# Kernel optimization log

Hardware: AMD Instinct MI355X
Metric: run time of the kernel (lower is better)

The kernel has to match this reference:

```python
import jax, jax.numpy as jnp
import numpy as np

B, H, F, T = 256, 1024, 512, 128  # batch, state_size, num_feature, num_predict

def setup_inputs() -> dict:
    key = jax.random.key(0)
    ks = jax.random.split(key, 8)
    s = 1.0 / np.sqrt(H)
    return {
        "x0": jax.random.normal(ks[0], (B, H), jnp.float32),
        "h0": jax.random.normal(ks[1], (B, H), jnp.float32),
        "c0": jax.random.normal(ks[2], (B, H), jnp.float32),
        "W": jax.random.uniform(ks[3], (H, 4 * H), jnp.float32, -s, s),   # input kernel (i,f,g,o)
        "U": jax.random.uniform(ks[4], (H, 4 * H), jnp.float32, -s, s),   # recurrent kernel
        "b": jnp.zeros((4 * H,), jnp.float32),
        "Wd": jax.random.uniform(ks[5], (H, F), jnp.float32, -s, s),      # Dense emission
        "bd": jnp.zeros((F,), jnp.float32),
    }

def _lstm_scan(x0, h0, c0, W, U, b):
    def step(carry, _):
        x, h, c = carry
        z = x @ W + h @ U + b                      # [B, 4H], Keras gate order i,f,g,o
        i, f, g, o = jnp.split(z, 4, axis=-1)
        c_new = jax.nn.sigmoid(f) * c + jax.nn.sigmoid(i) * jnp.tanh(g)
        h_new = jax.nn.sigmoid(o) * jnp.tanh(c_new)
        return (h_new, h_new, c_new), h_new       # output feeds back as next input
    (_, _, _), outs = jax.lax.scan(step, (x0, h0, c0), None, length=T)
    return outs                                    # [T, B, H]

def reference(x0, h0, c0, W, U, b, Wd, bd):
    outs = _lstm_scan(x0, h0, c0, W, U, b)         # [T, B, H]
    seq = jnp.transpose(outs, (1, 0, 2))           # [B, T, H]
    return seq @ Wd + bd                           # [B, T, F]
```

## Files before the change

### kernel.cpp

```cpp
#include <hip/hip_runtime.h>
#include <cstddef>
#include <cstdint>

typedef unsigned short ushort_t;
typedef __attribute__((ext_vector_type(8))) short bf16x8;
typedef __attribute__((ext_vector_type(4))) float f32x4;

#define Bb 256
#define Hh 1024
#define Ff 512
#define Tt 128

__device__ __forceinline__ ushort_t f2bf(float f) {
    unsigned int u = __float_as_uint(f);
    unsigned int r = (u + 0x7FFFu + ((u >> 16) & 1u)) >> 16;
    return (ushort_t)r;
}
__device__ __forceinline__ float sigf(float x)  { return 1.0f / (1.0f + __expf(-x)); }
__device__ __forceinline__ float tanhf_(float x){ return 2.0f / (1.0f + __expf(-2.0f * x)) - 1.0f; }

__device__ __forceinline__ void lds_barrier() {
    asm volatile("s_waitcnt lgkmcnt(0)" ::: "memory");
    __builtin_amdgcn_s_barrier();
    asm volatile("" ::: "memory");
}

__global__ void swz(const float* __restrict__ s0, const float* __restrict__ s1,
                    ushort_t* __restrict__ dst, int K, int N, int mode, int total)
{
    int KB = K >> 5;
    for (int idx = blockIdx.x * blockDim.x + threadIdx.x; idx < total;
         idx += gridDim.x * blockDim.x) {
        int blk   = idx >> 9;
        int lane  = (idx >> 3) & 63;
        int j     = idx & 7;
        int ntile = blk / KB;
        int kstep = blk - ntile * KB;
        int k = (kstep << 5) + ((lane >> 4) << 3) + j;
        int n;
        if (mode == 2) n = (ntile << 4) + (lane & 15);
        else           n = ((ntile & 3) << 10) + ((ntile >> 2) << 4) + (lane & 15);
        float v;
        if (mode == 0)      v = s0[(size_t)k * N + n] + s1[(size_t)k * N + n];
        else if (mode == 1) v = (k < 1024) ? s0[(size_t)k * N + n]
                                           : s1[(size_t)(k - 1024) * N + n];
        else                v = s0[(size_t)k * N + n];
        dst[idx] = f2bf(v);
    }
}

__global__ void mk_a0(const float* __restrict__ x0, const float* __restrict__ h0,
                      ushort_t* __restrict__ a0)
{
    int idx = blockIdx.x * blockDim.x + threadIdx.x;
    if (idx >= Bb * 2048) return;
    int r = idx >> 11, k = idx & 2047;
    float v = (k < 1024) ? x0[r * 1024 + k] : h0[r * 1024 + k - 1024];
    a0[idx] = f2bf(v);
}

__global__ void zero_bar(int* bar) {
    int i = blockIdx.x * blockDim.x + threadIdx.x;
    if (i < 1024) bar[i] = 0;
}


__global__ __launch_bounds__(256) void lstm_step(
    const ushort_t* __restrict__ Ap, int K,
    const ushort_t* __restrict__ Bw,
    const float* cin, float* cout,
    ushort_t* __restrict__ seqt,
    const float* __restrict__ bias)
{
    __shared__ __align__(16) ushort_t lA[32 * 512];
    __shared__ __align__(16) ushort_t lB[32 * 512];

    const int tid = threadIdx.x, w = tid >> 6, lane = tid & 63;
    const int id = blockIdx.x;
    const int ntg = ((id & 7) << 3) | (id >> 5);
    const int bt  = (id >> 3) & 3;
    const int r0 = bt << 6, hb = ntg << 4;
    const int wr = w >> 1, wc = w & 1;
    const int KB = K >> 5;

    f32x4 acc[2][2];
    #pragma unroll
    for (int m = 0; m < 2; ++m)
        #pragma unroll
        for (int n = 0; n < 2; ++n) acc[m][n] = (f32x4){0.f, 0.f, 0.f, 0.f};

    const int kp = tid & 31;
    const int q_a = kp & 3, kk_a = kp >> 2;

    for (int kc = 0; kc < K; kc += 256) {
        bf16x8 va[8];
        #pragma unroll
        for (int i = 0; i < 8; ++i) {
            int row = (i << 3) + (tid >> 5);
            va[i] = *(const bf16x8*)(Ap + (size_t)(r0 + row) * K + kc + (kp << 3));
        }
        bf16x8 vb[8];
        #pragma unroll
        for (int i = 0; i < 8; ++i)
            vb[i] = *(const bf16x8*)(Bw +
                ((((size_t)((ntg << 2) + w)) * KB + (kc >> 5) + i) << 9) + (lane << 3));
        #pragma unroll
        for (int i = 0; i < 8; ++i) {
            int row = (i << 3) + (tid >> 5);
            int msub = row >> 4, mm = row & 15;
            int pos = (q_a << 4) | (mm ^ (((kk_a << 2) + q_a) & 15));
            *(bf16x8*)&lA[((((kk_a << 2) + msub) << 6) + pos) << 3] = va[i];
        }
        #pragma unroll
        for (int i = 0; i < 8; ++i)
            *(bf16x8*)&lB[(((i << 2) + w) << 9) + (lane << 3)] = vb[i];
        __syncthreads();

        #pragma unroll
        for (int kk = 0; kk < 8; ++kk) {
            const int qq = lane >> 4, mm = lane & 15;
            const int pos = (qq << 4) | (mm ^ (((kk << 2) + qq) & 15));
            bf16x8 af[2], bfr[2];
            #pragma unroll
            for (int m = 0; m < 2; ++m)
                af[m] = *(const bf16x8*)&lA[((((kk << 2) + (wr << 1) + m) << 6) + pos) << 3];
            #pragma unroll
            for (int n = 0; n < 2; ++n)
                bfr[n] = *(const bf16x8*)&lB[((((kk << 2) + (wc << 1) + n) << 6) + lane) << 3];
            #pragma unroll
            for (int m = 0; m < 2; ++m)
                #pragma unroll
                for (int n = 0; n < 2; ++n)
                    acc[m][n] = __builtin_amdgcn_mfma_f32_16x16x32_bf16(
                        af[m], bfr[n], acc[m][n], 0, 0, 0);
        }
        __syncthreads();
    }

    float* lZ = (float*)lA;
    {
        int q = lane >> 4, nl = lane & 15;
        #pragma unroll
        for (int m = 0; m < 2; ++m)
            #pragma unroll
            for (int n = 0; n < 2; ++n)
                #pragma unroll
                for (int r = 0; r < 4; ++r)
                    lZ[((wr << 5) + (m << 4) + (q << 2) + r) * 68 +
                       (wc << 5) + (n << 4) + nl] = acc[m][n][r];
    }
    __syncthreads();

    #pragma unroll
    for (int i = 0; i < 4; ++i) {
        int idx = (i << 8) + tid;
        int row = idx >> 4, u = idx & 15;
        float zi = lZ[row * 68 +      u] + bias[       hb + u];
        float zf = lZ[row * 68 + 16 + u] + bias[1024 + hb + u];
        float zg = lZ[row * 68 + 32 + u] + bias[2048 + hb + u];
        float zo = lZ[row * 68 + 48 + u] + bias[3072 + hb + u];
        size_t cidx = (size_t)(r0 + row) * Hh + hb + u;
        float cp = cin[cidx];
        float cn = sigf(zf) * cp + sigf(zi) * tanhf_(zg);
        cout[cidx] = cn;
        seqt[cidx] = f2bf(sigf(zo) * tanhf_(cn));
    }
}

__global__ __launch_bounds__(256, 1) void lstm_scan(
    ushort_t* __restrict__ seq,
    const ushort_t* __restrict__ Msum,
    const float* __restrict__ bias,
    const float* __restrict__ cin,
    int* __restrict__ bar)
{
    __shared__ __align__(16) ushort_t lA[8][4096];

    const int tid = threadIdx.x, w = tid >> 6, lane = tid & 63;
    const int id = blockIdx.x;
    const int g  = id & 7;
    const int s  = id >> 3;
    const int r0 = g << 5;
    const int hb = s << 5;
    int* const barw = &bar[g << 5];

    bf16x8 Brg[2][32];
    #pragma unroll
    for (int n = 0; n < 2; ++n) {
        const int ntl = (w << 1) + n;
        const int gnt = (((s << 1) + (ntl >> 2)) << 2) + (ntl & 3);
        const ushort_t* bp = Msum + (((size_t)gnt << 5) << 9) + (lane << 3);
        #pragma unroll
        for (int ks = 0; ks < 32; ++ks) {
            Brg[n][ks] = *(const bf16x8*)(bp + ((size_t)ks << 9));
            asm volatile("" : "+a"(Brg[n][ks]));
        }
    }

    const int grow = tid >> 3, gu4 = (tid & 7) << 2;
    float c_reg[4], bi[4], bfv[4], bgv[4], bo[4];
    #pragma unroll
    for (int j = 0; j < 4; ++j) {
        int u = gu4 + j;
        c_reg[j] = cin[(size_t)(r0 + grow) * Hh + hb + u];
        bi[j]  = bias[       hb + u];
        bfv[j] = bias[1024 + hb + u];
        bgv[j] = bias[2048 + hb + u];
        bo[j]  = bias[3072 + hb + u];
    }

    float* lZ = (float*)lA;

    const int kp  = tid & 15;
    const int q_a = kp & 3, kk_a = kp >> 2;
    const int mm_s  = tid >> 4;
    const int pos_s = (q_a << 4) | (mm_s ^ (((kk_a << 2) + q_a) & 15));
    const int lw0   = (((kk_a << 1) << 6) | pos_s) << 3;
    const size_t ga0 = (size_t)(r0 + mm_s) * Hh + (kp << 3);

    #pragma unroll 1
    for (int t = 1; t < Tt; ++t) {
        const ushort_t* Ap = seq + ((size_t)(t - 1) << 18) + ga0;

        f32x4 acc[2][2];
        #pragma unroll
        for (int m = 0; m < 2; ++m)
            #pragma unroll
            for (int n = 0; n < 2; ++n) acc[m][n] = (f32x4){0.f, 0.f, 0.f, 0.f};

        bf16x8 rA[8][2];
        #pragma unroll
        for (int c = 0; c < 8; ++c)
            #pragma unroll
            for (int i = 0; i < 2; ++i)
                rA[c][i] = *(const bf16x8*)(Ap + (i << 14) + (c << 7));

        #pragma unroll
        for (int c = 0; c < 8; ++c)
            #pragma unroll
            for (int i = 0; i < 2; ++i)
                *(bf16x8*)&lA[c][lw0 + (i << 9)] = rA[c][i];
        lds_barrier();

        {
            const int qq = lane >> 4, mr = lane & 15;
            #pragma unroll
            for (int kc = 0; kc < 8; ++kc) {
                const ushort_t* lAc = lA[kc];
                #pragma unroll
                for (int kk = 0; kk < 4; ++kk) {
                    const int pos = (qq << 4) | (mr ^ (((kk << 2) + qq) & 15));
                    const int ks = (kc << 2) + kk;
                    bf16x8 af0 = *(const bf16x8*)&lAc[((((kk << 1) + 0) << 6) | pos) << 3];
                    bf16x8 af1 = *(const bf16x8*)&lAc[((((kk << 1) + 1) << 6) | pos) << 3];
                    acc[0][0] = __builtin_amdgcn_mfma_f32_16x16x32_bf16(af0, Brg[0][ks], acc[0][0], 0, 0, 0);
                    acc[0][1] = __builtin_amdgcn_mfma_f32_16x16x32_bf16(af0, Brg[1][ks], acc[0][1], 0, 0, 0);
                    acc[1][0] = __builtin_amdgcn_mfma_f32_16x16x32_bf16(af1, Brg[0][ks], acc[1][0], 0, 0, 0);
                    acc[1][1] = __builtin_amdgcn_mfma_f32_16x16x32_bf16(af1, Brg[1][ks], acc[1][1], 0, 0, 0);
                }
            }
        }
        lds_barrier();

        {
            const int q = lane >> 4, nl = lane & 15;
            #pragma unroll
            for (int m = 0; m < 2; ++m)
                #pragma unroll
                for (int n = 0; n < 2; ++n)
                    #pragma unroll
                    for (int r = 0; r < 4; ++r) {
                        int row = (m << 4) + (q << 2) + r;
                        int col = (((w << 1) + n) << 4) + nl;
                        lZ[(row << 7) + ((col + row * 5) & 127)] = acc[m][n][r];
                    }
        }
        lds_barrier();

        {
            const int rb5 = grow * 5;
            unsigned long long pk = 0;
            #pragma unroll
            for (int j = 0; j < 4; ++j) {
                int u = gu4 + j;
                int cb = ((u >> 4) << 6) + (u & 15);
                float zi = lZ[(grow << 7) + ((cb      + rb5) & 127)] + bi[j];
                float zf = lZ[(grow << 7) + ((cb + 16 + rb5) & 127)] + bfv[j];
                float zg = lZ[(grow << 7) + ((cb + 32 + rb5) & 127)] + bgv[j];
                float zo = lZ[(grow << 7) + ((cb + 48 + rb5) & 127)] + bo[j];
                float cn = sigf(zf) * c_reg[j] + sigf(zi) * tanhf_(zg);
                c_reg[j] = cn;
                pk |= (unsigned long long)f2bf(sigf(zo) * tanhf_(cn)) << (j << 4);
            }
            __hip_atomic_exchange(
                (unsigned long long*)&seq[((size_t)t << 18) +
                                          (size_t)(r0 + grow) * Hh + hb + gu4],
                pk, __ATOMIC_RELAXED, __HIP_MEMORY_SCOPE_AGENT);
        }

        if (t < Tt - 1) {
            __syncthreads();
            if (tid == 0) {
                __hip_atomic_fetch_add(barw, 1, __ATOMIC_RELAXED,
                                       __HIP_MEMORY_SCOPE_AGENT);
                int guard = 0;
                while (__hip_atomic_fetch_add(barw, 0, __ATOMIC_RELAXED,
                                              __HIP_MEMORY_SCOPE_AGENT) < (t << 5)
                       && ++guard < 30000)
                    __builtin_amdgcn_s_sleep(2);
            }
            lds_barrier();
        }
    }
}

__global__ __launch_bounds__(256) void emit(
    const ushort_t* __restrict__ seq,
    const ushort_t* __restrict__ Wsw,
    const float* __restrict__ bd,
    float* __restrict__ out)
{
    __shared__ __align__(16) ushort_t lA[2 * 8 * 64 * 8];
    __shared__ __align__(16) ushort_t lB[2 * 8 * 64 * 8];
    const int tid = threadIdx.x, w = tid >> 6, lane = tid & 63;
    const int id = blockIdx.x;
    const int rt = ((id >> 5) << 3) | (id & 7);
    const int ct = (id >> 3) & 3;
    const int r0 = rt << 7, f0 = ct << 7;
    const int wr = w >> 1, wc = w & 1;

    f32x4 acc[4][4];
    #pragma unroll
    for (int m = 0; m < 4; ++m)
        #pragma unroll
        for (int n = 0; n < 4; ++n) acc[m][n] = (f32x4){0.f, 0.f, 0.f, 0.f};

    for (int kc = 0; kc < Hh; kc += 64) {
        #pragma unroll
        for (int i = 0; i < 4; ++i) {
            int p = (i << 8) + tid;
            int row = p >> 3, kpp = p & 7;
            bf16x8 v = *(const bf16x8*)(seq + (size_t)(r0 + row) * Hh + kc + (kpp << 3));
            int kk = kpp >> 2, q = kpp & 3, msub = row >> 4, mm = row & 15;
            int pos = (q << 4) | (mm ^ (((kk << 2) + q) & 15));
            *(bf16x8*)&lA[((((kk << 3) + msub) << 6) + pos) << 3] = v;
        }
        #pragma unroll
        for (int i = 0; i < 4; ++i) {
            int d = (i << 8) + tid;
            int kk = d >> 9, csub = (d >> 6) & 7, ln = d & 63;
            int nt = (ct << 3) + csub;
            bf16x8 v = *(const bf16x8*)(Wsw + (((size_t)(nt * 32 + (kc >> 5) + kk)) << 9) + (ln << 3));
            *(bf16x8*)&lB[d << 3] = v;
        }
        __syncthreads();
        const int qq = lane >> 4, mm = lane & 15;
        #pragma unroll
        for (int kk = 0; kk < 2; ++kk) {
            const int pos = (qq << 4) | (mm ^ (((kk << 2) + qq) & 15));
            bf16x8 af[4], bfr[4];
            #pragma unroll
            for (int m = 0; m < 4; ++m)
                af[m] = *(const bf16x8*)&lA[((((kk << 3) + (wr << 2) + m) << 6) + pos) << 3];
            #pragma unroll
            for (int n = 0; n < 4; ++n)
                bfr[n] = *(const bf16x8*)&lB[((((kk << 3) + (wc << 2) + n) << 6) + lane) << 3];
            #pragma unroll
            for (int m = 0; m < 4; ++m)
                #pragma unroll
                for (int n = 0; n < 4; ++n)
                    acc[m][n] = __builtin_amdgcn_mfma_f32_16x16x32_bf16(
                        af[m], bfr[n], acc[m][n], 0, 0, 0);
        }
        __syncthreads();
    }

    int q = lane >> 4, nl = lane & 15;
    float bdv[4];
    #pragma unroll
    for (int n = 0; n < 4; ++n) bdv[n] = bd[f0 + (wc << 6) + (n << 4) + nl];
    #pragma unroll
    for (int m = 0; m < 4; ++m)
        #pragma unroll
        for (int r = 0; r < 4; ++r) {
            int grow2 = r0 + (wr << 6) + (m << 4) + (q << 2) + r;
            int tt = grow2 >> 8, bb = grow2 & 255;
            float* op = out + ((size_t)((bb << 7) + tt) << 9);
            #pragma unroll
            for (int n = 0; n < 4; ++n)
                op[f0 + (wc << 6) + (n << 4) + nl] = acc[m][n][r] + bdv[n];
        }
}

extern "C" void kernel_launch(void* const* d_in, const int* in_sizes, int n_in,
                              void* d_out, int out_size, void* d_ws, size_t ws_size,
                              hipStream_t stream)
{
    const float* x0 = (const float*)d_in[0];
    const float* h0 = (const float*)d_in[1];
    const float* c0 = (const float*)d_in[2];
    const float* W  = (const float*)d_in[3];
    const float* U  = (const float*)d_in[4];
    const float* b  = (const float*)d_in[5];
    const float* Wd = (const float*)d_in[6];
    const float* bd = (const float*)d_in[7];
    float* out = (float*)d_out;

    const size_t OFF_MCAT = 0;
    const size_t OFF_MSUM = 16777216;
    const size_t OFF_WSW  = 25165824;
    const size_t OFF_A0   = 26214400;
    const size_t OFF_SEQ  = 27262976;
    const size_t OFF_BAR  = 94371840;
    const size_t WS_NEED  = 94375936;
    if (ws_size < WS_NEED) return;

    char* ws = (char*)d_ws;
    ushort_t* Mcat = (ushort_t*)(ws + OFF_MCAT);
    ushort_t* Msum = (ushort_t*)(ws + OFF_MSUM);
    ushort_t* Wsw  = (ushort_t*)(ws + OFF_WSW);
    ushort_t* A0   = (ushort_t*)(ws + OFF_A0);
    ushort_t* seq  = (ushort_t*)(ws + OFF_SEQ);
    int*      bar  = (int*)(ws + OFF_BAR);
    float* cws = out;

    zero_bar<<<4, 256, 0, stream>>>(bar);
    mk_a0<<<2048, 256, 0, stream>>>(x0, h0, A0);
    swz<<<4096, 256, 0, stream>>>(W, U, Mcat, 2048, 4096, 1, 2048 * 4096);
    swz<<<2048, 256, 0, stream>>>(W, U, Msum, 1024, 4096, 0, 1024 * 4096);
    swz<<<512, 256, 0, stream>>>(Wd, nullptr, Wsw, 1024, 512, 2, 1024 * 512);

    lstm_step<<<256, 256, 0, stream>>>(A0, 2048, Mcat, c0, cws, seq, b);
    lstm_scan<<<256, 256, 0, stream>>>(seq, Msum, b, cws, bar);

    emit<<<1024, 256, 0, stream>>>(seq, Wsw, bd, out);
}
```

Baseline: 727.2 us.

## Split recurrent GEMM over K across waves and reduce partials in LDS

Each wave now covers all eight N tiles for one quarter of the K dimension instead of two N tiles over the full K. Partial sums go to a separate per-wave LDS region, and the gate epilogue adds the four partials with vectorized f32x4 loads. Because the partial buffer no longer aliases the A tile, the barrier between the MFMA loop and the partial write is removed. In exchange the kernel uses 64KB more LDS, does an extra reduction pass, and holds more accumulator registers per wave.

New measurement: 751.4 us. +3.3%, slower.

```diff
diff --git a/kernel.cpp b/kernel.cpp
--- a/kernel.cpp
+++ b/kernel.cpp
@@ -175,6 +175,7 @@
     int* __restrict__ bar)
 {
     __shared__ __align__(16) ushort_t lA[8][4096];
+    __shared__ __align__(16) float    lZp[16384];
 
     const int tid = threadIdx.x, w = tid >> 6, lane = tid & 63;
     const int id = blockIdx.x;
@@ -184,16 +185,15 @@
     const int hb = s << 5;
     int* const barw = &bar[g << 5];
 
-    bf16x8 Brg[2][32];
-    #pragma unroll
-    for (int n = 0; n < 2; ++n) {
-        const int ntl = (w << 1) + n;
+    bf16x8 Brg[8][8];
+    #pragma unroll
+    for (int ntl = 0; ntl < 8; ++ntl) {
         const int gnt = (((s << 1) + (ntl >> 2)) << 2) + (ntl & 3);
-        const ushort_t* bp = Msum + (((size_t)gnt << 5) << 9) + (lane << 3);
-        #pragma unroll
-        for (int ks = 0; ks < 32; ++ks) {
-            Brg[n][ks] = *(const bf16x8*)(bp + ((size_t)ks << 9));
-            asm volatile("" : "+a"(Brg[n][ks]));
+        const ushort_t* bp = Msum + (((size_t)((gnt << 5) + (w << 3))) << 9) + (lane << 3);
+        #pragma unroll
+        for (int kl = 0; kl < 8; ++kl) {
+            Brg[ntl][kl] = *(const bf16x8*)(bp + ((size_t)kl << 9));
+            asm volatile("" : "+a"(Brg[ntl][kl]));
         }
     }
 
@@ -209,8 +209,6 @@
         bo[j]  = bias[3072 + hb + u];
     }
 
-    float* lZ = (float*)lA;
-
     const int kp  = tid & 15;
     const int q_a = kp & 3, kk_a = kp >> 2;
     const int mm_s  = tid >> 4;
@@ -218,15 +216,18 @@
     const int lw0   = (((kk_a << 1) << 6) | pos_s) << 3;
     const size_t ga0 = (size_t)(r0 + mm_s) * Hh + (kp << 3);
 
+    const int cb = ((gu4 >> 4) << 6) + (gu4 & 15);
+    const int rb4 = grow << 2;
+
     #pragma unroll 1
     for (int t = 1; t < Tt; ++t) {
         const ushort_t* Ap = seq + ((size_t)(t - 1) << 18) + ga0;
 
-        f32x4 acc[2][2];
+        f32x4 acc[2][8];
         #pragma unroll
         for (int m = 0; m < 2; ++m)
             #pragma unroll
-            for (int n = 0; n < 2; ++n) acc[m][n] = (f32x4){0.f, 0.f, 0.f, 0.f};
+            for (int ntl = 0; ntl < 8; ++ntl) acc[m][ntl] = (f32x4){0.f, 0.f, 0.f, 0.f};
 
         bf16x8 rA[8][2];
         #pragma unroll
@@ -245,49 +246,53 @@
         {
             const int qq = lane >> 4, mr = lane & 15;
             #pragma unroll
-            for (int kc = 0; kc < 8; ++kc) {
-                const ushort_t* lAc = lA[kc];
+            for (int kl = 0; kl < 8; ++kl) {
+                const int kk = kl & 3;
+                const ushort_t* lAc = lA[(w << 1) + (kl >> 2)];
+                const int pos = (qq << 4) | (mr ^ (((kk << 2) + qq) & 15));
+                bf16x8 af0 = *(const bf16x8*)&lAc[((((kk << 1) + 0) << 6) | pos) << 3];
+                bf16x8 af1 = *(const bf16x8*)&lAc[((((kk << 1) + 1) << 6) | pos) << 3];
                 #pragma unroll
-                for (int kk = 0; kk < 4; ++kk) {
-                    const int pos = (qq << 4) | (mr ^ (((kk << 2) + qq) & 15));
-                    const int ks = (kc << 2) + kk;
-                    bf16x8 af0 = *(const bf16x8*)&lAc[((((kk << 1) + 0) << 6) | pos) << 3];
-                    bf16x8 af1 = *(const bf16x8*)&lAc[((((kk << 1) + 1) << 6) | pos) << 3];
-                    acc[0][0] = __builtin_amdgcn_mfma_f32_16x16x32_bf16(af0, Brg[0][ks], acc[0][0], 0, 0, 0);
-                    acc[0][1] = __builtin_amdgcn_mfma_f32_16x16x32_bf16(af0, Brg[1][ks], acc[0][1], 0, 0, 0);
-                    acc[1][0] = __builtin_amdgcn_mfma_f32_16x16x32_bf16(af1, Brg[0][ks], acc[1][0], 0, 0, 0);
-                    acc[1][1] = __builtin_amdgcn_mfma_f32_16x16x32_bf16(af1, Brg[1][ks], acc[1][1], 0, 0, 0);
+                for (int ntl = 0; ntl < 8; ++ntl) {
+                    acc[0][ntl] = __builtin_amdgcn_mfma_f32_16x16x32_bf16(af0, Brg[ntl][kl], acc[0][ntl], 0, 0, 0);
+                    acc[1][ntl] = __builtin_amdgcn_mfma_f32_16x16x32_bf16(af1, Brg[ntl][kl], acc[1][ntl], 0, 0, 0);
                 }
             }
         }
-        lds_barrier();
 
         {
             const int q = lane >> 4, nl = lane & 15;
+            float* zw = &lZp[w << 12];
             #pragma unroll
             for (int m = 0; m < 2; ++m)
                 #pragma unroll
-                for (int n = 0; n < 2; ++n)
+                for (int ntl = 0; ntl < 8; ++ntl)
                     #pragma unroll
                     for (int r = 0; r < 4; ++r) {
                         int row = (m << 4) + (q << 2) + r;
-                        int col = (((w << 1) + n) << 4) + nl;
-                        lZ[(row << 7) + ((col + row * 5) & 127)] = acc[m][n][r];
+                        int col = (ntl << 4) + nl;
+                        zw[(row << 7) + ((col + (row << 2)) & 127)] = acc[m][ntl][r];
                     }
         }
         lds_barrier();
 
         {
-            const int rb5 = grow * 5;
+            f32x4 vi = (f32x4){0.f,0.f,0.f,0.f}, vf = vi, vg = vi, vo = vi;
+            #pragma unroll
+            for (int p = 0; p < 4; ++p) {
+                const float* zp = &lZp[(p << 12) + (grow << 7)];
+                vi += *(const f32x4*)&zp[(cb      + rb4) & 127];
+                vf += *(const f32x4*)&zp[(cb + 16 + rb4) & 127];
+                vg += *(const f32x4*)&zp[(cb + 32 + rb4) & 127];
+                vo += *(const f32x4*)&zp[(cb + 48 + rb4) & 127];
+            }
             unsigned long long pk = 0;
             #pragma unroll
             for (int j = 0; j < 4; ++j) {
-                int u = gu4 + j;
-                int cb = ((u >> 4) << 6) + (u & 15);
-                float zi = lZ[(grow << 7) + ((cb      + rb5) & 127)] + bi[j];
-                float zf = lZ[(grow << 7) + ((cb + 16 + rb5) & 127)] + bfv[j];
-                float zg = lZ[(grow << 7) + ((cb + 32 + rb5) & 127)] + bgv[j];
-                float zo = lZ[(grow << 7) + ((cb + 48 + rb5) & 127)] + bo[j];
+                float zi = vi[j] + bi[j];
+                float zf = vf[j] + bfv[j];
+                float zg = vg[j] + bgv[j];
+                float zo = vo[j] + bo[j];
                 float cn = sigf(zf) * c_reg[j] + sigf(zi) * tanhf_(zg);
                 c_reg[j] = cn;
                 pk |= (unsigned long long)f2bf(sigf(zo) * tanhf_(cn)) << (j << 4);
```
